# Kernel tuning notes

Measured on AMD Instinct MI355X. Metric: run time of the kernel, lower is better.

Reference implementation:

```python
import jax, jax.numpy as jnp
import numpy as np
import math

B, L, E, H = 4, 2048, 1024, 16
HD = E // H
SIGMA = 10.0
ATTN_BIAS = 0.1  # source bug: dropout_p=0.1 is passed as attn_mask and added to scores


def setup_inputs() -> dict:
    key = jax.random.key(0)
    ks = jax.random.split(key, 6)
    return {
        "query": jax.random.normal(ks[0], (B, L, E), jnp.float32),
        "key": jax.random.normal(ks[1], (B, L, E), jnp.float32),
        "value": jax.random.normal(ks[2], (B, L, E), jnp.float32),
        "gauss": jax.random.uniform(ks[3], (B * H // 2, L), jnp.float32),
        "in_proj_weight": jax.random.normal(ks[4], (3 * E, E), jnp.float32) * (1.0 / math.sqrt(E)),
        "in_proj_bias": jnp.zeros((3 * E,), jnp.float32),
        "out_proj_weight": jax.random.normal(ks[5], (E, E), jnp.float32) * (1.0 / math.sqrt(E)),
        "out_proj_bias": jnp.zeros((E,), jnp.float32),
    }


def reference(query, key, value, gauss, in_proj_weight, in_proj_bias,
              out_proj_weight, out_proj_bias):
    # packed in-projection (q,k,v distinct tensors -> chunk weights in 3)
    wq, wk, wv = jnp.split(in_proj_weight, 3, axis=0)   # each [E, E]
    bq, bk, bv = jnp.split(in_proj_bias, 3, axis=0)
    q = query @ wq.T + bq          # [B, L, E]
    k = key @ wk.T + bk
    v = value @ wv.T + bv

    def split_heads(x):            # [B, L, E] -> [B*H, L, HD], index = b*H + h
        return x.reshape(B, L, H, HD).transpose(0, 2, 1, 3).reshape(B * H, L, HD)

    q, k, v = split_heads(q), split_heads(k), split_heads(v)
    q = q * (1.0 / math.sqrt(HD))

    attn = jnp.einsum("bnd,bmd->bnm", q, k) + ATTN_BIAS   # [B*H, L, L]
    gw = jnp.exp(-gauss * SIGMA)                          # [B*H//2, L]
    # even/odd batch rows share the same gaussian row -> pairwise broadcast
    attn = (attn.reshape(B * H // 2, 2, L, L) * gw[:, None, None, :]).reshape(B * H, L, L)
    attn = jax.nn.softmax(attn, axis=-1)

    out = jnp.einsum("bnm,bmd->bnd", attn, v)             # [B*H, L, HD]
    out = out.reshape(B, H, L, HD).transpose(0, 2, 1, 3).reshape(B, L, E)
    return out @ out_proj_weight.T + out_proj_bias        # [B, L, E]
```

## Files before the change

kernel.cpp:

```cpp
#include <hip/hip_runtime.h>
#include <stdint.h>
#include <stddef.h>


typedef __attribute__((ext_vector_type(8))) short bf16x8;
typedef __attribute__((ext_vector_type(4))) float f32x4;

__device__ __forceinline__ unsigned short f2b(float f) {
  unsigned int u = __builtin_bit_cast(unsigned int, f);
  u += 0x7FFFu + ((u >> 16) & 1u);
  return (unsigned short)(u >> 16);
}
__device__ __forceinline__ bf16x8 cvt8(f32x4 a, f32x4 b) {
  bf16x8 r;
#pragma unroll
  for (int i = 0; i < 4; ++i) { r[i] = (short)f2b(a[i]); r[4 + i] = (short)f2b(b[i]); }
  return r;
}
__device__ __forceinline__ bf16x8 pk8(f32x4 a, f32x4 b) {
  union { bf16x8 v; unsigned int w[4]; } u;
  asm("v_cvt_pk_bf16_f32 %0, %1, %2" : "=v"(u.w[0]) : "v"(a[0]), "v"(a[1]));
  asm("v_cvt_pk_bf16_f32 %0, %1, %2" : "=v"(u.w[1]) : "v"(a[2]), "v"(a[3]));
  asm("v_cvt_pk_bf16_f32 %0, %1, %2" : "=v"(u.w[2]) : "v"(b[0]), "v"(b[1]));
  asm("v_cvt_pk_bf16_f32 %0, %1, %2" : "=v"(u.w[3]) : "v"(b[2]), "v"(b[3]));
  return u.v;
}
__device__ __forceinline__ float fexp2(float x) { return __builtin_amdgcn_exp2f(x); }

#define GLD16(gp, lp) __builtin_amdgcn_global_load_lds( \
  (const __attribute__((address_space(1))) void*)(gp), \
  (__attribute__((address_space(3))) void*)(lp), 16, 0, 0)

#define FBAR() do { \
  asm volatile("" ::: "memory"); \
  __builtin_amdgcn_sched_barrier(0); \
  __builtin_amdgcn_s_barrier(); \
  __builtin_amdgcn_sched_barrier(0); \
  asm volatile("" ::: "memory"); \
} while (0)

__global__ void __launch_bounds__(256) gw_exp_kernel(const float* __restrict__ g,
                                                     float* __restrict__ gtab,
                                                     float* __restrict__ btab, int n) {
  int i = blockIdx.x * 256 + threadIdx.x;
  if (i < n) {
    const float e = __expf(g[i] * -10.0f) * 1.44269504f;
    gtab[i] = e;
    btab[i] = 0.1f * e;
  }
}

__global__ void __launch_bounds__(256) conv_bf16_kernel(
    const float* __restrict__ w1, const float* __restrict__ w2,
    unsigned short* __restrict__ dst)
{
  const size_t i = ((size_t)blockIdx.x * 256 + threadIdx.x) * 8;
  const float* s; size_t off;
  if (i < ((size_t)3 << 20)) { s = w1; off = i; }
  else                       { s = w2; off = i - ((size_t)3 << 20); }
  const f32x4 a = *(const f32x4*)(s + off);
  const f32x4 b = *(const f32x4*)(s + off + 4);
  *(bf16x8*)(dst + i) = cvt8(a, b);
}

template<int EPI>
__global__ void __launch_bounds__(512, 2) gemm8p(
    const float* __restrict__ Aq, const float* __restrict__ Ak,
    const float* __restrict__ Av, const unsigned short* __restrict__ Abf,
    const unsigned short* __restrict__ Bw,
    const float* __restrict__ bias, const float* __restrict__ gtab,
    unsigned short* __restrict__ Qo, unsigned short* __restrict__ Ko,
    unsigned short* __restrict__ Vto, float* __restrict__ Co,
    int N, int K, int nTN)
{
  const int nwg = gridDim.x;
  const int cpx = nwg >> 3;
  const int bid2 = (blockIdx.x & 7) * cpx + (blockIdx.x >> 3);
  const int tm = bid2 / nTN, tn = bid2 % nTN;

  __shared__ __align__(16) char lds[2][49152];

  const int tid = threadIdx.x;
  const int w = tid >> 6, l = tid & 63;
  const int lr = l & 15, lg = l >> 4;
  const int wm = w >> 2, wn = w & 3;
  const size_t Kz = (size_t)K;

  const int r0 = tid >> 3;
  const int e0 = (((tid & 7) ^ ((tid >> 3) & 7)) << 3);
  const size_t arow0 = (size_t)(tm * 128 + r0);
  const size_t brow0 = (size_t)(tn * 256 + r0);

  const float* Af = (tn >> 2) == 0 ? Aq : ((tn >> 2) == 1 ? Ak : Av);

  f32x4 ar0[4], ar1[4];
  auto ldA = [&](f32x4* ar, int k0) {
    const float* pa = Af + arow0 * Kz + k0 + e0;
    const float* pb = Af + (arow0 + 64) * Kz + k0 + e0;
    ar[0] = *(const __attribute__((address_space(1))) f32x4*)pa;
    ar[1] = *(const __attribute__((address_space(1))) f32x4*)(pa + 4);
    ar[2] = *(const __attribute__((address_space(1))) f32x4*)pb;
    ar[3] = *(const __attribute__((address_space(1))) f32x4*)(pb + 4);
  };
  auto wrA = [&](f32x4* ar, int s) {
    *(bf16x8*)&lds[s][tid * 16]        = pk8(ar[0], ar[1]);
    *(bf16x8*)&lds[s][8192 + tid * 16] = pk8(ar[2], ar[3]);
  };
  auto stAbf = [&](int s, int k0) {
    GLD16(Abf + arow0 * Kz + k0 + e0,        &lds[s][tid * 16]);
    GLD16(Abf + (arow0 + 64) * Kz + k0 + e0, &lds[s][8192 + tid * 16]);
  };
  auto stB = [&](int s, int h, int k0) {
    const size_t rb = brow0 + h * 128;
    GLD16(Bw + rb * Kz + k0 + e0,        &lds[s][16384 + h * 16384 + tid * 16]);
    GLD16(Bw + (rb + 64) * Kz + k0 + e0, &lds[s][16384 + h * 16384 + 8192 + tid * 16]);
  };

  int offA[4][2], offB[4][2];
#pragma unroll
  for (int m = 0; m < 4; ++m) {
    const int ra = wm * 64 + m * 16 + lr;
#pragma unroll
    for (int kk = 0; kk < 2; ++kk)
      offA[m][kk] = ra * 128 + ((((kk << 2) | lg) ^ (ra & 7)) << 4);
  }
#pragma unroll
  for (int n = 0; n < 4; ++n) {
    const int br = wn * 64 + n * 16 + lr;
    const int lrow = br & 127;
#pragma unroll
    for (int kk = 0; kk < 2; ++kk)
      offB[n][kk] = 16384 + (br >> 7) * 16384 + lrow * 128 +
                    ((((kk << 2) | lg) ^ (lrow & 7)) << 4);
  }

  f32x4 acc[4][4];
  const f32x4 zero = {0.f, 0.f, 0.f, 0.f};
#pragma unroll
  for (int i = 0; i < 4; ++i)
#pragma unroll
    for (int j = 0; j < 4; ++j) acc[i][j] = zero;

  bf16x8 af[2][2], bf[4][2];

  auto loadA = [&](const char* Ls, int mh) {
#pragma unroll
    for (int mm = 0; mm < 2; ++mm)
#pragma unroll
      for (int kk = 0; kk < 2; ++kk)
        af[mm][kk] = *(const bf16x8*)(Ls + offA[mh * 2 + mm][kk]);
  };
  auto loadB = [&](const char* Ls) {
#pragma unroll
    for (int n = 0; n < 4; ++n)
#pragma unroll
      for (int kk = 0; kk < 2; ++kk)
        bf[n][kk] = *(const bf16x8*)(Ls + offB[n][kk]);
  };
  auto mfmaq = [&](int mh) {
    asm volatile("s_waitcnt lgkmcnt(0)" ::: "memory");
    __builtin_amdgcn_sched_barrier(0);
    __builtin_amdgcn_s_setprio(1);
#pragma unroll
    for (int mm = 0; mm < 2; ++mm)
#pragma unroll
      for (int n = 0; n < 4; ++n) {
        f32x4 a = acc[mh * 2 + mm][n];
        a = __builtin_amdgcn_mfma_f32_16x16x32_bf16(af[mm][0], bf[n][0], a, 0, 0, 0);
        a = __builtin_amdgcn_mfma_f32_16x16x32_bf16(af[mm][1], bf[n][1], a, 0, 0, 0);
        acc[mh * 2 + mm][n] = a;
      }
    __builtin_amdgcn_s_setprio(0);
  };

  const char* L0 = (const char*)lds[0];
  const char* L1 = (const char*)lds[1];

  if constexpr (EPI == 0) { ldA(ar0, 0); } else { stAbf(0, 0); }
  stB(0, 0, 0); stB(0, 1, 0);

  const int NI = K / 128;
  for (int i = 0; i < NI; ++i) {
    const int k1 = i * 128 + 64;
    const int k2 = i * 128 + 128;
    if constexpr (EPI == 0) {
      ldA(ar1, k1); stB(1, 0, k1);
      asm volatile("s_waitcnt vmcnt(6)" ::: "memory");
      wrA(ar0, 0);
      asm volatile("s_waitcnt lgkmcnt(0)" ::: "memory");
    } else {
      stAbf(1, k1); stB(1, 0, k1);
      asm volatile("s_waitcnt vmcnt(4)" ::: "memory");
    }
    FBAR();
    loadA(L0, 0); loadB(L0);
    mfmaq(0);
    FBAR();
    stB(1, 1, k1);
    loadA(L0, 1);
    mfmaq(1);
    FBAR();
    if constexpr (EPI == 0) {
      if (i + 1 < NI) {
        ldA(ar0, k2); stB(0, 0, k2);
        asm volatile("s_waitcnt vmcnt(6)" ::: "memory");
      } else {
        asm volatile("s_waitcnt vmcnt(0)" ::: "memory");
      }
      wrA(ar1, 1);
      asm volatile("s_waitcnt lgkmcnt(0)" ::: "memory");
    } else {
      if (i + 1 < NI) {
        stAbf(0, k2); stB(0, 0, k2);
        asm volatile("s_waitcnt vmcnt(4)" ::: "memory");
      } else {
        asm volatile("s_waitcnt vmcnt(0)" ::: "memory");
      }
    }
    FBAR();
    loadA(L1, 0); loadB(L1);
    mfmaq(0);
    FBAR();
    if (i + 1 < NI) stB(0, 1, k2);
    loadA(L1, 1);
    mfmaq(1);
    FBAR();
  }

  if (EPI == 0 && (tn >> 2) == 2) {
    __syncthreads();
    char* T = &lds[0][0];
#pragma unroll
    for (int n = 0; n < 4; ++n) {
      const int cnl = wn * 64 + n * 16 + lr;
      const float bv = bias[tn * 256 + cnl];
      const int sw = (cnl & 7) << 4;
#pragma unroll
      for (int m = 0; m < 4; ++m)
#pragma unroll
        for (int r = 0; r < 4; ++r) {
          const int rml = wm * 64 + m * 16 + lg * 4 + r;
          *(unsigned short*)(T + cnl * 256 + ((rml * 2) ^ sw)) = f2b(acc[m][n][r] + bv);
        }
    }
    __syncthreads();
    const int bbase = (tm >> 4) * 16 + (tn - 8) * 4;
    const size_t ncol = (size_t)(tm & 15) * 128;
#pragma unroll
    for (int rep = 0; rep < 8; ++rep) {
      const int U = rep * 512 + tid;
      const int row = U >> 4;
      const int un = U & 15;
      const bf16x8 vv = *(const bf16x8*)(T + row * 256 + ((un * 16) ^ ((row & 7) << 4)));
      const int bh = bbase + (row >> 6);
      const int d = row & 63;
      *(bf16x8*)(Vto + ((size_t)bh * 64 + d) * 2048 + ncol + un * 8) = vv;
    }
  } else {
#pragma unroll
    for (int n = 0; n < 4; ++n) {
      const int cn = tn * 256 + wn * 64 + n * 16 + lr;
      const float bv = bias[cn];
      const int j = cn & 1023;
      const float* gK = nullptr;
      if constexpr (EPI == 0) {
        if ((tn >> 2) == 1) {
          const int bh_ = (tm >> 4) * 16 + (j >> 6);
          gK = gtab + (size_t)(bh_ >> 1) * 2048;
        }
      }
#pragma unroll
      for (int m = 0; m < 4; ++m) {
        const int rm0 = tm * 128 + wm * 64 + m * 16 + lg * 4;
        f32x4 g4;
        if constexpr (EPI == 0) {
          if (gK) g4 = *(const f32x4*)&gK[rm0 & 2047];
        }
#pragma unroll
        for (int r = 0; r < 4; ++r) {
          const int rm = rm0 + r;
          const float val = acc[m][n][r] + bv;
          if constexpr (EPI == 0) {
            const int bh = (rm >> 11) * 16 + (j >> 6);
            const int d = j & 63;
            const int nr = rm & 2047;
            if ((tn >> 2) == 0) Qo[((size_t)bh * 2048 + nr) * 64 + d] = f2b(val * 0.125f);
            else                Ko[((size_t)bh * 2048 + nr) * 64 + d] = f2b(val * g4[r]);
          } else {
            Co[(size_t)rm * N + cn] = val;
          }
        }
      }
    }
  }
}

__global__ void __launch_bounds__(256, 2) attn_kernel(
    const unsigned short* __restrict__ Q, const unsigned short* __restrict__ Kf,
    const unsigned short* __restrict__ Vt, const float* __restrict__ btab,
    unsigned short* __restrict__ O)
{
  const int bid2 = (blockIdx.x & 7) * 64 + (blockIdx.x >> 3);
  const int bh = bid2 >> 3;
  const int qb = bid2 & 7;
  const int tid = threadIdx.x;
  const int w = tid >> 6, l = tid & 63;
  const int lr = l & 15, lg = l >> 4;

  __shared__ __align__(16) unsigned short Kl[2][64 * 64];
  __shared__ __align__(16) unsigned short Vl[2][64 * 64];

  const int qrow = qb * 256 + w * 64 + lr;
  const unsigned short* qp = &Q[((size_t)bh * 2048 + qrow) * 64];
  bf16x8 aq[4][2];
#pragma unroll
  for (int st = 0; st < 4; ++st) {
    aq[st][0] = *(const bf16x8*)&qp[st * 16 * 64 + lg * 8];
    aq[st][1] = *(const bf16x8*)&qp[st * 16 * 64 + 32 + lg * 8];
  }

  const f32x4 zero = {0.f, 0.f, 0.f, 0.f};
  f32x4 accO[4][4];
  f32x4 lsum[4];
#pragma unroll
  for (int st = 0; st < 4; ++st) {
    lsum[st] = zero;
#pragma unroll
    for (int dt = 0; dt < 4; ++dt) accO[st][dt] = zero;
  }

  const short oneb = (short)0x3F80;
  const bf16x8 vones = {oneb, oneb, oneb, oneb, oneb, oneb, oneb, oneb};

  int off[4][2];
#pragma unroll
  for (int mt = 0; mt < 4; ++mt)
#pragma unroll
    for (int c = 0; c < 2; ++c) {
      const int rr = mt * 16 + lr;
      off[mt][c] = rr * 128 + ((((c << 2) + lg) ^ (rr & 7)) << 4);
    }

  const int rr0 = w * 8 + (l >> 3);
  const int cc = ((l & 7) ^ (rr0 & 7)) * 8;
  const int kk0 = (rr0 & 35) | ((rr0 & 12) << 1) | ((rr0 & 16) >> 2);
  const unsigned short* kSrc = &Kf[((size_t)bh * 2048 + kk0) * 64 + cc];
  const unsigned short* vSrc = &Vt[((size_t)bh * 64 + rr0) * 2048 + cc];

  auto stageKV = [&](int buf) {
    GLD16(kSrc,             &Kl[buf][w * 512]);
    GLD16(kSrc + 32 * 64,   &Kl[buf][(w + 4) * 512]);
    GLD16(vSrc,             &Vl[buf][w * 512]);
    GLD16(vSrc + 32 * 2048, &Vl[buf][(w + 4) * 512]);
    kSrc += 64 * 64;
    vSrc += 64;
  };

  const float* brow = &btab[(size_t)(bh >> 1) * 2048];

  stageKV(0);
  for (int t = 0; t < 32; ++t) {
    __syncthreads();
    if (t + 1 < 32) stageKV((t + 1) & 1);
    const char* kl = (const char*)Kl[t & 1];
    const char* vl = (const char*)Vl[t & 1];

    bf16x8 ap[4][2];
#pragma unroll
    for (int half = 0; half < 2; ++half) {
      f32x4 s[4][2];
      __builtin_amdgcn_s_setprio(1);
#pragma unroll
      for (int mh = 0; mh < 2; ++mh) {
        const int mt = half * 2 + mh;
        const bf16x8 bk0 = *(const bf16x8*)(kl + off[mt][0]);
        const bf16x8 bk1 = *(const bf16x8*)(kl + off[mt][1]);
        const f32x4 b4 = *(const f32x4*)&brow[t * 64 + (half << 5) + (lg << 3) + (mh << 2)];
#pragma unroll
        for (int st = 0; st < 4; ++st) {
          f32x4 a = __builtin_amdgcn_mfma_f32_16x16x32_bf16(bk0, aq[st][0], b4, 0, 0, 0);
          a = __builtin_amdgcn_mfma_f32_16x16x32_bf16(bk1, aq[st][1], a, 0, 0, 0);
          s[st][mh] = a;
        }
      }
      __builtin_amdgcn_s_setprio(0);
#pragma unroll
      for (int st = 0; st < 4; ++st) {
#pragma unroll
        for (int mh = 0; mh < 2; ++mh)
#pragma unroll
          for (int r = 0; r < 4; ++r) s[st][mh][r] = fexp2(s[st][mh][r]);
        ap[st][half] = pk8(s[st][0], s[st][1]);
      }
    }

    __builtin_amdgcn_s_setprio(1);
#pragma unroll
    for (int st = 0; st < 4; ++st) {
      lsum[st] = __builtin_amdgcn_mfma_f32_16x16x32_bf16(ap[st][0], vones, lsum[st], 0, 0, 0);
      lsum[st] = __builtin_amdgcn_mfma_f32_16x16x32_bf16(ap[st][1], vones, lsum[st], 0, 0, 0);
    }
#pragma unroll
    for (int dt = 0; dt < 4; ++dt) {
      const bf16x8 bv0 = *(const bf16x8*)(vl + off[dt][0]);
      const bf16x8 bv1 = *(const bf16x8*)(vl + off[dt][1]);
#pragma unroll
      for (int st = 0; st < 4; ++st) {
        f32x4 a = accO[st][dt];
        a = __builtin_amdgcn_mfma_f32_16x16x32_bf16(ap[st][0], bv0, a, 0, 0, 0);
        a = __builtin_amdgcn_mfma_f32_16x16x32_bf16(ap[st][1], bv1, a, 0, 0, 0);
        accO[st][dt] = a;
      }
    }
    __builtin_amdgcn_s_setprio(0);
  }

  const int oc0 = (bh & 15) * 64;
#pragma unroll
  for (int st = 0; st < 4; ++st) {
    const int orow0 = (bh >> 4) * 2048 + qb * 256 + w * 64 + st * 16 + lg * 4;
    f32x4 rc;
#pragma unroll
    for (int r = 0; r < 4; ++r) rc[r] = 1.0f / lsum[st][r];
#pragma unroll
    for (int dt = 0; dt < 4; ++dt)
#pragma unroll
      for (int r = 0; r < 4; ++r)
        O[(size_t)(orow0 + r) * 1024 + oc0 + dt * 16 + lr] = f2b(accO[st][dt][r] * rc[r]);
  }
}

extern "C" void kernel_launch(void* const* d_in, const int* in_sizes, int n_in,
                              void* d_out, int out_size, void* d_ws, size_t ws_size,
                              hipStream_t stream) {
  (void)in_sizes; (void)n_in; (void)out_size; (void)ws_size;
  const float* query = (const float*)d_in[0];
  const float* key_  = (const float*)d_in[1];
  const float* value = (const float*)d_in[2];
  const float* gauss = (const float*)d_in[3];
  const float* ipw   = (const float*)d_in[4];
  const float* ipb   = (const float*)d_in[5];
  const float* opw   = (const float*)d_in[6];
  const float* opb   = (const float*)d_in[7];

  char* ws = (char*)d_ws;
  unsigned short* W1  = (unsigned short*)ws;
  unsigned short* W2  = W1 + ((size_t)3 << 20);
  unsigned short* AO  = W1 + ((size_t)4 << 20);
  unsigned short* Qf  = W1 + ((size_t)12 << 20);
  unsigned short* Kf  = Qf + ((size_t)8 << 20);
  unsigned short* Vt  = Kf + ((size_t)8 << 20);
  float*          gtab = (float*)(Vt + ((size_t)8 << 20));
  float*          btab = gtab + 32 * 2048;

  gw_exp_kernel<<<256, 256, 0, stream>>>(gauss, gtab, btab, 32 * 2048);

  conv_bf16_kernel<<<2048, 256, 0, stream>>>(ipw, opw, W1);

  gemm8p<0><<<64 * 12, 512, 0, stream>>>(
      query, key_, value, nullptr, W1, ipb, gtab,
      Qf, Kf, Vt, nullptr, 3072, 1024, 12);

  attn_kernel<<<512, 256, 0, stream>>>(Qf, Kf, Vt, btab, AO);

  gemm8p<1><<<64 * 4, 512, 0, stream>>>(
      nullptr, nullptr, nullptr, AO, W2, opb, nullptr,
      nullptr, nullptr, nullptr, (float*)d_out, 1024, 1024, 4);
}
```

Measured before the change: 189.3 us.

## Deepen fp32 A-operand prefetch and move LDS writes into mid-phase slots

In the fp32-input GEMM path, A register loads now run one extra 64-wide K chunk ahead, using two register sets (even and odd chunks). The bf16 conversion and LDS write of A is moved into the middle of each phase, after the first MFMA half, instead of sitting just before a barrier with a blocking lgkmcnt wait. This is meant to hide global-load latency and take the conversion stall off the critical path before each barrier. It costs more live registers, and the hand-tuned vmcnt counts must stay correct or LDS data races appear.

```diff
diff --git a/kernel.cpp b/kernel.cpp
--- a/kernel.cpp
+++ b/kernel.cpp
@@ -93,7 +93,7 @@
 
   const float* Af = (tn >> 2) == 0 ? Aq : ((tn >> 2) == 1 ? Ak : Av);
 
-  f32x4 ar0[4], ar1[4];
+  f32x4 arE[4], arO[4];
   auto ldA = [&](f32x4* ar, int k0) {
     const float* pa = Af + arow0 * Kz + k0 + e0;
     const float* pb = Af + (arow0 + 64) * Kz + k0 + e0;
@@ -176,18 +176,33 @@
   const char* L0 = (const char*)lds[0];
   const char* L1 = (const char*)lds[1];
 
-  if constexpr (EPI == 0) { ldA(ar0, 0); } else { stAbf(0, 0); }
-  stB(0, 0, 0); stB(0, 1, 0);
-
   const int NI = K / 128;
+
+  if constexpr (EPI == 0) {
+    ldA(arE, 0);
+    ldA(arO, 64);
+    stB(0, 0, 0); stB(0, 1, 0);
+    asm volatile("s_waitcnt vmcnt(8)" ::: "memory");
+    wrA(arE, 0);
+    asm volatile("s_waitcnt lgkmcnt(0)" ::: "memory");
+  } else {
+    stAbf(0, 0);
+    stB(0, 0, 0); stB(0, 1, 0);
+  }
+
   for (int i = 0; i < NI; ++i) {
     const int k1 = i * 128 + 64;
     const int k2 = i * 128 + 128;
+    const int k3 = i * 128 + 192;
     if constexpr (EPI == 0) {
-      ldA(ar1, k1); stB(1, 0, k1);
-      asm volatile("s_waitcnt vmcnt(6)" ::: "memory");
-      wrA(ar0, 0);
-      asm volatile("s_waitcnt lgkmcnt(0)" ::: "memory");
+      if (i + 1 < NI) {
+        ldA(arE, k2);
+        stB(1, 0, k1);
+        asm volatile("s_waitcnt vmcnt(6)" ::: "memory");
+      } else {
+        stB(1, 0, k1);
+        asm volatile("s_waitcnt vmcnt(2)" ::: "memory");
+      }
     } else {
       stAbf(1, k1); stB(1, 0, k1);
       asm volatile("s_waitcnt vmcnt(4)" ::: "memory");
@@ -197,18 +212,18 @@
     mfmaq(0);
     FBAR();
     stB(1, 1, k1);
+    if constexpr (EPI == 0) wrA(arO, 1);
     loadA(L0, 1);
     mfmaq(1);
     FBAR();
     if constexpr (EPI == 0) {
       if (i + 1 < NI) {
-        ldA(ar0, k2); stB(0, 0, k2);
+        ldA(arO, k3);
+        stB(0, 0, k2);
         asm volatile("s_waitcnt vmcnt(6)" ::: "memory");
       } else {
         asm volatile("s_waitcnt vmcnt(0)" ::: "memory");
       }
-      wrA(ar1, 1);
-      asm volatile("s_waitcnt lgkmcnt(0)" ::: "memory");
     } else {
       if (i + 1 < NI) {
         stAbf(0, k2); stB(0, 0, k2);
@@ -221,7 +236,10 @@
     loadA(L1, 0); loadB(L1);
     mfmaq(0);
     FBAR();
-    if (i + 1 < NI) stB(0, 1, k2);
+    if (i + 1 < NI) {
+      stB(0, 1, k2);
+      if constexpr (EPI == 0) wrA(arE, 0);
+    }
     loadA(L1, 1);
     mfmaq(1);
     FBAR();
```

After: 190.1 us. No clear change (+0.4%).

## Split in-projection into dedicated GEMM with smaller tiles and 3-stage LDS pipeline

Applied to the files above, without the earlier changes.

Replaces the templated in-projection GEMM with a dedicated kernel that uses 128x128 tiles, BK=32, and a triple-buffered LDS ring. The fp32 activation tile is loaded straight into LDS through async global_load_lds and converted to bf16 when fragments are read, instead of going through registers. Occupancy goes to 4 workgroups per CU and the grid doubles to 1536 blocks. The aim is better latency hiding and wave balance for the in-projection. The cost is less data reuse per tile, twice the LDS bytes per A element, and conversion work in the inner loop.

```diff
diff --git a/kernel.cpp b/kernel.cpp
--- a/kernel.cpp
+++ b/kernel.cpp
@@ -30,14 +30,6 @@
 #define GLD16(gp, lp) __builtin_amdgcn_global_load_lds( \
   (const __attribute__((address_space(1))) void*)(gp), \
   (__attribute__((address_space(3))) void*)(lp), 16, 0, 0)
-
-#define FBAR() do { \
-  asm volatile("" ::: "memory"); \
-  __builtin_amdgcn_sched_barrier(0); \
-  __builtin_amdgcn_s_barrier(); \
-  __builtin_amdgcn_sched_barrier(0); \
-  asm volatile("" ::: "memory"); \
-} while (0)
 
 __global__ void __launch_bounds__(256) gw_exp_kernel(const float* __restrict__ g,
                                                      float* __restrict__ gtab,
@@ -63,21 +55,155 @@
   *(bf16x8*)(dst + i) = cvt8(a, b);
 }
 
-template<int EPI>
-__global__ void __launch_bounds__(512, 2) gemm8p(
+__global__ void __launch_bounds__(512, 4) gemm_ip(
     const float* __restrict__ Aq, const float* __restrict__ Ak,
-    const float* __restrict__ Av, const unsigned short* __restrict__ Abf,
-    const unsigned short* __restrict__ Bw,
+    const float* __restrict__ Av, const unsigned short* __restrict__ Bw,
     const float* __restrict__ bias, const float* __restrict__ gtab,
     unsigned short* __restrict__ Qo, unsigned short* __restrict__ Ko,
-    unsigned short* __restrict__ Vto, float* __restrict__ Co,
-    int N, int K, int nTN)
+    unsigned short* __restrict__ Vto, int K, int nTN)
 {
   const int nwg = gridDim.x;
   const int cpx = nwg >> 3;
   const int bid2 = (blockIdx.x & 7) * cpx + (blockIdx.x >> 3);
   const int tm = bid2 / nTN, tn = bid2 % nTN;
 
+  __shared__ __align__(16) char lds[3][24576];
+
+  const int tid = threadIdx.x;
+  const int w = tid >> 6, l = tid & 63;
+  const int lr = l & 15, lg = l >> 4;
+  const size_t Kz = (size_t)K;
+
+  const float* Af = tn < 8 ? Aq : (tn < 16 ? Ak : Av);
+
+  auto stage = [&](int buf, int kt) {
+    const int k0 = kt * 32;
+#pragma unroll
+    for (int j = 0; j < 2; ++j) {
+      const int u = j * 512 + tid;
+      const int rr = u >> 3;
+      const int ce = ((u & 7) ^ (rr & 7)) << 2;
+      GLD16(Af + (size_t)(tm * 128 + rr) * Kz + k0 + ce, &lds[buf][u * 16]);
+    }
+    const int rb = tid >> 2;
+    const int cb = ((tid & 3) ^ ((rb >> 1) & 3)) << 3;
+    GLD16(Bw + (size_t)(tn * 128 + rb) * Kz + k0 + cb, &lds[buf][16384 + tid * 16]);
+  };
+
+  f32x4 acc[4][2];
+  const f32x4 zero = {0.f, 0.f, 0.f, 0.f};
+#pragma unroll
+  for (int i = 0; i < 4; ++i)
+#pragma unroll
+    for (int j = 0; j < 2; ++j) acc[i][j] = zero;
+
+  const int wr = (w >> 2) * 64, wc = (w & 3) * 32;
+  const int NT = K / 32;
+
+  stage(0, 0);
+  stage(1, 1);
+  int rbuf = 0, wbuf = 2;
+  for (int kt = 0; kt < NT; ++kt) {
+    if (kt == NT - 1) { asm volatile("s_waitcnt vmcnt(0)" ::: "memory"); }
+    else              { asm volatile("s_waitcnt vmcnt(3)" ::: "memory"); }
+    __builtin_amdgcn_sched_barrier(0);
+    __builtin_amdgcn_s_barrier();
+    __builtin_amdgcn_sched_barrier(0);
+    if (kt + 2 < NT) stage(wbuf, kt + 2);
+    const char* la = lds[rbuf];
+    const char* lb = lds[rbuf] + 16384;
+    bf16x8 af[4], bfr[2];
+#pragma unroll
+    for (int mi = 0; mi < 4; ++mi) {
+      const int ra = wr + mi * 16 + lr;
+      const f32x4 lo = *(const f32x4*)(la + ra * 128 + ((((lg << 1))     ^ (ra & 7)) << 4));
+      const f32x4 hi = *(const f32x4*)(la + ra * 128 + ((((lg << 1) | 1) ^ (ra & 7)) << 4));
+      af[mi] = pk8(lo, hi);
+    }
+#pragma unroll
+    for (int ni = 0; ni < 2; ++ni) {
+      const int rb2 = wc + ni * 16 + lr;
+      bfr[ni] = *(const bf16x8*)(lb + rb2 * 64 + ((lg ^ ((rb2 >> 1) & 3)) << 4));
+    }
+#pragma unroll
+    for (int mi = 0; mi < 4; ++mi)
+#pragma unroll
+      for (int ni = 0; ni < 2; ++ni)
+        acc[mi][ni] = __builtin_amdgcn_mfma_f32_16x16x32_bf16(
+            af[mi], bfr[ni], acc[mi][ni], 0, 0, 0);
+    rbuf = (rbuf == 2) ? 0 : rbuf + 1;
+    wbuf = (wbuf == 2) ? 0 : wbuf + 1;
+  }
+
+  if (tn >= 16) {
+    __syncthreads();
+    char* T = &lds[0][0];
+#pragma unroll
+    for (int ni = 0; ni < 2; ++ni) {
+      const int cnl = wc + ni * 16 + lr;
+      const float bv = bias[tn * 128 + cnl];
+#pragma unroll
+      for (int mi = 0; mi < 4; ++mi)
+#pragma unroll
+        for (int r = 0; r < 4; ++r) {
+          const int rml = wr + mi * 16 + lg * 4 + r;
+          const int byte = cnl * 256 + (((rml * 2)) ^ ((cnl & 3) << 5));
+          *(unsigned short*)(T + byte) = f2b(acc[mi][ni][r] + bv);
+        }
+    }
+    __syncthreads();
+    const int bbase = (tm >> 4) * 16 + (tn - 16) * 2;
+    const size_t ncol = (size_t)(tm & 15) * 128;
+#pragma unroll
+    for (int rep = 0; rep < 4; ++rep) {
+      const int U = rep * 512 + tid;
+      const int row = U >> 4;
+      const int un = U & 15;
+      const bf16x8 vv = *(const bf16x8*)(T + row * 256 + ((un * 16) ^ ((row & 3) << 5)));
+      const int bh = bbase + (row >> 6);
+      const int d = row & 63;
+      *(bf16x8*)(Vto + ((size_t)bh * 64 + d) * 2048 + ncol + un * 8) = vv;
+    }
+  } else {
+#pragma unroll
+    for (int ni = 0; ni < 2; ++ni) {
+      const int cn = tn * 128 + wc + ni * 16 + lr;
+      const float bv = bias[cn];
+      const int j = cn & 1023;
+      const float* gK = nullptr;
+      if (tn >= 8) {
+        const int bh_ = (tm >> 4) * 16 + (j >> 6);
+        gK = gtab + (size_t)(bh_ >> 1) * 2048;
+      }
+#pragma unroll
+      for (int mi = 0; mi < 4; ++mi) {
+        const int rm0 = tm * 128 + wr + mi * 16 + lg * 4;
+        f32x4 g4;
+        if (gK) g4 = *(const f32x4*)&gK[rm0 & 2047];
+#pragma unroll
+        for (int r = 0; r < 4; ++r) {
+          const int rm = rm0 + r;
+          const float val = acc[mi][ni][r] + bv;
+          const int bh = (rm >> 11) * 16 + (j >> 6);
+          const int d = j & 63;
+          const int nr = rm & 2047;
+          if (tn < 8) Qo[((size_t)bh * 2048 + nr) * 64 + d] = f2b(val * 0.125f);
+          else        Ko[((size_t)bh * 2048 + nr) * 64 + d] = f2b(val * g4[r]);
+        }
+      }
+    }
+  }
+}
+
+__global__ void __launch_bounds__(512, 2) gemm_op(
+    const unsigned short* __restrict__ Abf, const unsigned short* __restrict__ Bw,
+    const float* __restrict__ bias, float* __restrict__ Co, int N, int K, int nTN)
+{
+  const int nwg = gridDim.x;
+  const int cpx = nwg >> 3;
+  const int bid2 = (blockIdx.x & 7) * cpx + (blockIdx.x >> 3);
+  const int tm = bid2 / nTN, tn = bid2 % nTN;
+
   __shared__ __align__(16) char lds[2][49152];
 
   const int tid = threadIdx.x;
@@ -91,22 +217,7 @@
   const size_t arow0 = (size_t)(tm * 128 + r0);
   const size_t brow0 = (size_t)(tn * 256 + r0);
 
-  const float* Af = (tn >> 2) == 0 ? Aq : ((tn >> 2) == 1 ? Ak : Av);
-
-  f32x4 ar0[4], ar1[4];
-  auto ldA = [&](f32x4* ar, int k0) {
-    const float* pa = Af + arow0 * Kz + k0 + e0;
-    const float* pb = Af + (arow0 + 64) * Kz + k0 + e0;
-    ar[0] = *(const __attribute__((address_space(1))) f32x4*)pa;
-    ar[1] = *(const __attribute__((address_space(1))) f32x4*)(pa + 4);
-    ar[2] = *(const __attribute__((address_space(1))) f32x4*)pb;
-    ar[3] = *(const __attribute__((address_space(1))) f32x4*)(pb + 4);
-  };
-  auto wrA = [&](f32x4* ar, int s) {
-    *(bf16x8*)&lds[s][tid * 16]        = pk8(ar[0], ar[1]);
-    *(bf16x8*)&lds[s][8192 + tid * 16] = pk8(ar[2], ar[3]);
-  };
-  auto stAbf = [&](int s, int k0) {
+  auto stA = [&](int s, int k0) {
     GLD16(Abf + arow0 * Kz + k0 + e0,        &lds[s][tid * 16]);
     GLD16(Abf + (arow0 + 64) * Kz + k0 + e0, &lds[s][8192 + tid * 16]);
   };
@@ -173,25 +284,25 @@
     __builtin_amdgcn_s_setprio(0);
   };
 
+#define FBAR() do { \
+  asm volatile("" ::: "memory"); \
+  __builtin_amdgcn_sched_barrier(0); \
+  __builtin_amdgcn_s_barrier(); \
+  __builtin_amdgcn_sched_barrier(0); \
+  asm volatile("" ::: "memory"); \
+} while (0)
+
   const char* L0 = (const char*)lds[0];
   const char* L1 = (const char*)lds[1];
-
-  if constexpr (EPI == 0) { ldA(ar0, 0); } else { stAbf(0, 0); }
-  stB(0, 0, 0); stB(0, 1, 0);
-
   const int NI = K / 128;
+
+  stA(0, 0); stB(0, 0, 0); stB(0, 1, 0);
+
   for (int i = 0; i < NI; ++i) {
     const int k1 = i * 128 + 64;
     const int k2 = i * 128 + 128;
-    if constexpr (EPI == 0) {
-      ldA(ar1, k1); stB(1, 0, k1);
-      asm volatile("s_waitcnt vmcnt(6)" ::: "memory");
-      wrA(ar0, 0);
-      asm volatile("s_waitcnt lgkmcnt(0)" ::: "memory");
-    } else {
-      stAbf(1, k1); stB(1, 0, k1);
-      asm volatile("s_waitcnt vmcnt(4)" ::: "memory");
-    }
+    stA(1, k1); stB(1, 0, k1);
+    asm volatile("s_waitcnt vmcnt(4)" ::: "memory");
     FBAR();
     loadA(L0, 0); loadB(L0);
     mfmaq(0);
@@ -200,22 +311,11 @@
     loadA(L0, 1);
     mfmaq(1);
     FBAR();
-    if constexpr (EPI == 0) {
-      if (i + 1 < NI) {
-        ldA(ar0, k2); stB(0, 0, k2);
-        asm volatile("s_waitcnt vmcnt(6)" ::: "memory");
-      } else {
-        asm volatile("s_waitcnt vmcnt(0)" ::: "memory");
-      }
-      wrA(ar1, 1);
-      asm volatile("s_waitcnt lgkmcnt(0)" ::: "memory");
+    if (i + 1 < NI) {
+      stA(0, k2); stB(0, 0, k2);
+      asm volatile("s_waitcnt vmcnt(4)" ::: "memory");
     } else {
-      if (i + 1 < NI) {
-        stAbf(0, k2); stB(0, 0, k2);
-        asm volatile("s_waitcnt vmcnt(4)" ::: "memory");
-      } else {
-        asm volatile("s_waitcnt vmcnt(0)" ::: "memory");
-      }
+      asm volatile("s_waitcnt vmcnt(0)" ::: "memory");
     }
     FBAR();
     loadA(L1, 0); loadB(L1);
@@ -227,69 +327,16 @@
     FBAR();
   }
 
-  if (EPI == 0 && (tn >> 2) == 2) {
-    __syncthreads();
-    char* T = &lds[0][0];
-#pragma unroll
-    for (int n = 0; n < 4; ++n) {
-      const int cnl = wn * 64 + n * 16 + lr;
-      const float bv = bias[tn * 256 + cnl];
-      const int sw = (cnl & 7) << 4;
-#pragma unroll
-      for (int m = 0; m < 4; ++m)
-#pragma unroll
-        for (int r = 0; r < 4; ++r) {
-          const int rml = wm * 64 + m * 16 + lg * 4 + r;
-          *(unsigned short*)(T + cnl * 256 + ((rml * 2) ^ sw)) = f2b(acc[m][n][r] + bv);
-        }
-    }
-    __syncthreads();
-    const int bbase = (tm >> 4) * 16 + (tn - 8) * 4;
-    const size_t ncol = (size_t)(tm & 15) * 128;
-#pragma unroll
-    for (int rep = 0; rep < 8; ++rep) {
-      const int U = rep * 512 + tid;
-      const int row = U >> 4;
-      const int un = U & 15;
-      const bf16x8 vv = *(const bf16x8*)(T + row * 256 + ((un * 16) ^ ((row & 7) << 4)));
-      const int bh = bbase + (row >> 6);
-      const int d = row & 63;
-      *(bf16x8*)(Vto + ((size_t)bh * 64 + d) * 2048 + ncol + un * 8) = vv;
-    }
-  } else {
-#pragma unroll
-    for (int n = 0; n < 4; ++n) {
-      const int cn = tn * 256 + wn * 64 + n * 16 + lr;
-      const float bv = bias[cn];
-      const int j = cn & 1023;
-      const float* gK = nullptr;
-      if constexpr (EPI == 0) {
-        if ((tn >> 2) == 1) {
-          const int bh_ = (tm >> 4) * 16 + (j >> 6);
-          gK = gtab + (size_t)(bh_ >> 1) * 2048;
-        }
-      }
-#pragma unroll
-      for (int m = 0; m < 4; ++m) {
-        const int rm0 = tm * 128 + wm * 64 + m * 16 + lg * 4;
-        f32x4 g4;
-        if constexpr (EPI == 0) {
-          if (gK) g4 = *(const f32x4*)&gK[rm0 & 2047];
-        }
-#pragma unroll
-        for (int r = 0; r < 4; ++r) {
-          const int rm = rm0 + r;
-          const float val = acc[m][n][r] + bv;
-          if constexpr (EPI == 0) {
-            const int bh = (rm >> 11) * 16 + (j >> 6);
-            const int d = j & 63;
-            const int nr = rm & 2047;
-            if ((tn >> 2) == 0) Qo[((size_t)bh * 2048 + nr) * 64 + d] = f2b(val * 0.125f);
-            else                Ko[((size_t)bh * 2048 + nr) * 64 + d] = f2b(val * g4[r]);
-          } else {
-            Co[(size_t)rm * N + cn] = val;
-          }
-        }
+#pragma unroll
+  for (int n = 0; n < 4; ++n) {
+    const int cn = tn * 256 + wn * 64 + n * 16 + lr;
+    const float bv = bias[cn];
+#pragma unroll
+    for (int m = 0; m < 4; ++m) {
+#pragma unroll
+      for (int r = 0; r < 4; ++r) {
+        const int rm = tm * 128 + wm * 64 + m * 16 + lg * 4 + r;
+        Co[(size_t)rm * N + cn] = acc[m][n][r] + bv;
       }
     }
   }
@@ -457,13 +504,11 @@
 
   conv_bf16_kernel<<<2048, 256, 0, stream>>>(ipw, opw, W1);
 
-  gemm8p<0><<<64 * 12, 512, 0, stream>>>(
-      query, key_, value, nullptr, W1, ipb, gtab,
-      Qf, Kf, Vt, nullptr, 3072, 1024, 12);
+  gemm_ip<<<64 * 24, 512, 0, stream>>>(
+      query, key_, value, W1, ipb, gtab, Qf, Kf, Vt, 1024, 24);
 
   attn_kernel<<<512, 256, 0, stream>>>(Qf, Kf, Vt, btab, AO);
 
-  gemm8p<1><<<64 * 4, 512, 0, stream>>>(
-      nullptr, nullptr, nullptr, AO, W2, opb, nullptr,
-      nullptr, nullptr, nullptr, (float*)d_out, 1024, 1024, 4);
-}
+  gemm_op<<<64 * 4, 512, 0, stream>>>(
+      AO, W2, opb, (float*)d_out, 1024, 1024, 4);
+}
```

New measurement: 198.5 us. 1.05x slower.
